# Performance work log

Measured on AMD Instinct MI355X. Metric: run time of the kernel, lower is better.

Reference implementation:

```python
import jax, jax.numpy as jnp
import numpy as np

N_AGT, N_CTX, E, D, NC = 100000, 10000, 1000000, 128, 2


def _gn(x, w, b, eps=1e-5):
    # GroupNorm(num_groups=1) on (N, C): normalize over channels, affine.
    m = jnp.mean(x, axis=-1, keepdims=True)
    v = jnp.mean((x - m) ** 2, axis=-1, keepdims=True)
    return (x - m) * jax.lax.rsqrt(v + eps) * w + b


def setup_inputs() -> dict:
    key = jax.random.key(0)
    ks = jax.random.split(key, 16)
    s = 0.05  # weight scale
    return {
        "agts": jax.random.normal(ks[0], (N_AGT, D), jnp.float32),
        "ctx": jax.random.normal(ks[1], (N_CTX, D), jnp.float32),
        "agt_ctrs": jax.random.normal(ks[2], (N_AGT, NC), jnp.float32),
        "ctx_ctrs": jax.random.normal(ks[3], (N_CTX, NC), jnp.float32),
        "hi": jax.random.randint(ks[4], (E,), 0, N_AGT, jnp.int32),
        "wi": jax.random.randint(ks[5], (E,), 0, N_CTX, jnp.int32),
        "dist_w1": jax.random.normal(ks[6], (D, NC), jnp.float32) * s,
        "dist_b1": jnp.zeros((D,), jnp.float32),
        "dist_w2": jax.random.normal(ks[7], (D, D), jnp.float32) * s,
        "dist_gw": jnp.ones((D,), jnp.float32),
        "dist_gb": jnp.zeros((D,), jnp.float32),
        "q_w": jax.random.normal(ks[8], (D, D), jnp.float32) * s,
        "q_gw": jnp.ones((D,), jnp.float32),
        "q_gb": jnp.zeros((D,), jnp.float32),
        "ctx_w1": jax.random.normal(ks[9], (D, 3 * D), jnp.float32) * s,
        "ctx_gw": jnp.ones((D,), jnp.float32),
        "ctx_gb": jnp.zeros((D,), jnp.float32),
        "ctx_w2": jax.random.normal(ks[10], (D, D), jnp.float32) * s,
        "agt_w": jax.random.normal(ks[11], (D, D), jnp.float32) * s,
        "norm_gw": jnp.ones((D,), jnp.float32),
        "norm_gb": jnp.zeros((D,), jnp.float32),
        "lin_w": jax.random.normal(ks[12], (D, D), jnp.float32) * s,
        "lin_gw": jnp.ones((D,), jnp.float32),
        "lin_gb": jnp.zeros((D,), jnp.float32),
    }


def reference(agts, ctx, agt_ctrs, ctx_ctrs, hi, wi,
              dist_w1, dist_b1, dist_w2, dist_gw, dist_gb,
              q_w, q_gw, q_gb,
              ctx_w1, ctx_gw, ctx_gb, ctx_w2,
              agt_w, norm_gw, norm_gb,
              lin_w, lin_gw, lin_gb):
    res = agts
    # per-edge relative displacement: [E, 2]
    d = agt_ctrs[hi] - ctx_ctrs[wi]
    # dist MLP: Linear(2,128)+ReLU, Linear(128,128,nobias)+GN+ReLU
    d = jax.nn.relu(d @ dist_w1.T + dist_b1)
    d = jax.nn.relu(_gn(d @ dist_w2.T, dist_gw, dist_gb))
    # query: Linear(128,128,nobias)+GN+ReLU on gathered agents
    q = jax.nn.relu(_gn(agts[hi] @ q_w.T, q_gw, q_gb))
    # concat-MLP over edges: [E, 384] -> [E, 128]
    c = jnp.concatenate([d, q, ctx[wi]], axis=1)
    c = jax.nn.relu(_gn(c @ ctx_w1.T, ctx_gw, ctx_gb))
    c = c @ ctx_w2.T
    # agent transform + index_add scatter of edge messages
    a = agts @ agt_w.T
    a = a.at[hi].add(c)
    a = jax.nn.relu(_gn(a, norm_gw, norm_gb))
    a = _gn(a @ lin_w.T, lin_gw, lin_gb)  # Linear block with act=False
    a = jax.nn.relu(a + res)
    return a
```

## Files before the change

### kernel.cpp

```cpp
#include <hip/hip_runtime.h>
#include <stdint.h>


#define N_AGT 100000
#define N_CTX 10000
#define NE    1000000
#define D     128

typedef __attribute__((ext_vector_type(8))) __bf16 bf16x8;
typedef __attribute__((ext_vector_type(4))) float f32x4;
typedef __attribute__((ext_vector_type(4))) unsigned int uint32x4;
typedef __attribute__((ext_vector_type(8))) unsigned short ushort8;

__device__ __forceinline__ float bf_lo(uint32_t u){ return __uint_as_float(u << 16); }
__device__ __forceinline__ float bf_hi(uint32_t u){ return __uint_as_float(u & 0xFFFF0000u); }
__device__ __forceinline__ uint16_t f2bf(float f){
  uint32_t u = __float_as_uint(f);
  u += 0x7FFFu + ((u >> 16) & 1u);
  return (uint16_t)(u >> 16);
}
__device__ __forceinline__ float bf2f(uint16_t v){ return __uint_as_float(((uint32_t)v) << 16); }

__device__ __forceinline__ f32x4 mfma16(bf16x8 a, bf16x8 b, f32x4 c){
  return __builtin_amdgcn_mfma_f32_16x16x32_bf16(a, b, c, 0, 0, 0);
}

__device__ __forceinline__ void wave_lgkm0(){
  asm volatile("s_waitcnt lgkmcnt(0)" ::: "memory");
  __builtin_amdgcn_sched_barrier(0);
}


__device__ __forceinline__ void stage_wsz(char* dst, const float* __restrict__ W,
                                          int rs, int co, int tid, int nthr){
  for (int idx = tid; idx < 128*16; idx += nthr){
    const int row = idx >> 4, ch = idx & 15;
    const float4 f0 = *(const float4*)(W + (size_t)row*rs + co + ch*8);
    const float4 f1 = *(const float4*)(W + (size_t)row*rs + co + ch*8 + 4);
    ushort8 u;
    u[0]=f2bf(f0.x); u[1]=f2bf(f0.y); u[2]=f2bf(f0.z); u[3]=f2bf(f0.w);
    u[4]=f2bf(f1.x); u[5]=f2bf(f1.y); u[6]=f2bf(f1.z); u[7]=f2bf(f1.w);
    *(uint32x4*)(dst + row*256 + ((ch*16) ^ ((row&7)<<4))) = __builtin_bit_cast(uint32x4, u);
  }
}

__device__ __forceinline__ bf16x8 ldfrag(const char* base, int row, int cb){
  return __builtin_bit_cast(bf16x8,
      *(const uint32x4*)(base + row*256 + (cb ^ ((row&7)<<4))));
}

#define NWIT (NE/16)

__device__ __forceinline__ void mm16(const char* T, const char* W,
                                     int llo, int lhi, f32x4 acc[8]){
  bf16x8 a[4];
  #pragma unroll
  for (int kt = 0; kt < 4; kt++) a[kt] = ldfrag(T, llo, kt*64 + lhi*16);
  #pragma unroll
  for (int nt = 0; nt < 8; nt++){
    acc[nt] = (f32x4)0.f;
    #pragma unroll
    for (int kt = 0; kt < 4; kt++){
      const bf16x8 b = ldfrag(W, nt*16 + llo, kt*64 + lhi*16);
      acc[nt] = mfma16(a[kt], b, acc[nt]);
    }
  }
}

__device__ __forceinline__ void gn_reg(f32x4 acc[8], const float gw[8],
                                       const float gb[8]){
  float s[4] = {0,0,0,0}, ss[4] = {0,0,0,0};
  #pragma unroll
  for (int nt = 0; nt < 8; nt++)
    #pragma unroll
    for (int r = 0; r < 4; r++){
      const float v = acc[nt][r];
      s[r] += v; ss[r] += v*v;
    }
  #pragma unroll
  for (int m = 1; m < 16; m <<= 1)
    #pragma unroll
    for (int r = 0; r < 4; r++){
      s[r] += __shfl_xor(s[r], m);
      ss[r] += __shfl_xor(ss[r], m);
    }
  float mean[4], rstd[4];
  #pragma unroll
  for (int r = 0; r < 4; r++){
    mean[r] = s[r]*(1.f/128.f);
    const float var = ss[r]*(1.f/128.f) - mean[r]*mean[r];
    rstd[r] = rsqrtf(var + 1e-5f);
  }
  #pragma unroll
  for (int nt = 0; nt < 8; nt++)
    #pragma unroll
    for (int r = 0; r < 4; r++)
      acc[nt][r] = fmaxf((acc[nt][r]-mean[r])*rstd[r]*gw[nt] + gb[nt], 0.f);
}

__device__ __forceinline__ void scat16(char* T, const f32x4 acc[8],
                                       int llo, int lhi){
  #pragma unroll
  for (int nt = 0; nt < 8; nt++)
    #pragma unroll
    for (int r = 0; r < 4; r++){
      const int row = lhi*4 + r;
      *(uint16_t*)(T + row*256 + ((2*(nt*16 + llo)) ^ ((row&7)<<4))) =
          f2bf(acc[nt][r]);
    }
}

__global__ __launch_bounds__(512, 2) void k_edge_mfma(
    const float* __restrict__ agt_ctrs, const float* __restrict__ ctx_ctrs,
    const int* __restrict__ hi, const int* __restrict__ wi,
    const float* __restrict__ dist_w1, const float* __restrict__ dist_b1,
    const float* __restrict__ dist_gw, const float* __restrict__ dist_gb,
    const float* __restrict__ ctx_gw, const float* __restrict__ ctx_gb,
    const float* __restrict__ dist_w2, const float* __restrict__ ctx_w1,
    const float* __restrict__ ctx_w2,
    const uint16_t* __restrict__ QW, const uint16_t* __restrict__ CtxP,
    float* __restrict__ A0){
  extern __shared__ __align__(16) char smem[];
  const int tid  = threadIdx.x;
  const int wave = tid >> 6, lane = tid & 63;
  const int lhi  = lane >> 4, llo = lane & 15;

  stage_wsz(smem,         dist_w2, 128, 0, tid, 512);
  stage_wsz(smem + 32768, ctx_w1,  384, 0, tid, 512);
  stage_wsz(smem + 65536, ctx_w2,  128, 0, tid, 512);

  char* T = smem + 98304 + wave*4096;

  const int c0 = llo*8;
  float w1x[8], w1y[8], b1v[8];
  #pragma unroll
  for (int j = 0; j < 8; j++){
    w1x[j] = dist_w1[(c0+j)*2 + 0];
    w1y[j] = dist_w1[(c0+j)*2 + 1];
    b1v[j] = dist_b1[c0+j];
  }
  float dgwr[8], dgbr[8], cgwr[8], cgbr[8];
  #pragma unroll
  for (int nt = 0; nt < 8; nt++){
    dgwr[nt] = dist_gw[nt*16 + llo]; dgbr[nt] = dist_gb[nt*16 + llo];
    cgwr[nt] = ctx_gw[nt*16 + llo];  cgbr[nt] = ctx_gb[nt*16 + llo];
  }
  __syncthreads();

  const int wid = blockIdx.x*8 + wave;
  const int nw  = gridDim.x*8;

  for (int i = wid; i < NWIT; i += nw){
    const int base = i*16;
    const int4 h4 = *(const int4*)&hi[base + lhi*4];
    const int4 w4 = *(const int4*)&wi[base + lhi*4];
    const int hh[4] = {h4.x, h4.y, h4.z, h4.w};
    const int ww[4] = {w4.x, w4.y, w4.z, w4.w};
    const int h2 = hi[base + llo], w2 = wi[base + llo];
    uint32x4 qql[4], qcl[4];
    #pragma unroll
    for (int k = 0; k < 4; k++){
      qql[k] = *(const uint32x4*)&QW  [(size_t)h2*D + lhi*32 + k*8];
      qcl[k] = *(const uint32x4*)&CtxP[(size_t)w2*D + lhi*32 + k*8];
    }
    #pragma unroll
    for (int j = 0; j < 4; j++){
      const float2 ac = *(const float2*)&agt_ctrs[(size_t)hh[j]*2];
      const float2 cc = *(const float2*)&ctx_ctrs[(size_t)ww[j]*2];
      const float dx = ac.x - cc.x, dy = ac.y - cc.y;
      ushort8 u;
      #pragma unroll
      for (int c = 0; c < 8; c++)
        u[c] = f2bf(fmaxf(fmaf(dx, w1x[c], fmaf(dy, w1y[c], b1v[c])), 0.f));
      const int row = lhi*4 + j;
      *(uint32x4*)(T + row*256 + ((llo*16) ^ ((row&7)<<4))) =
          __builtin_bit_cast(uint32x4, u);
    }
    wave_lgkm0();
    f32x4 acc[8];
    mm16(T, smem, llo, lhi, acc);
    gn_reg(acc, dgwr, dgbr);
    wave_lgkm0();
    scat16(T, acc, llo, lhi);
    wave_lgkm0();
    mm16(T, smem + 32768, llo, lhi, acc);
    ushort8 qs[4];
    #pragma unroll
    for (int k = 0; k < 4; k++){
      const ushort8 a = __builtin_bit_cast(ushort8, qql[k]);
      const ushort8 b = __builtin_bit_cast(ushort8, qcl[k]);
      ushort8 v;
      #pragma unroll
      for (int j = 0; j < 8; j++) v[j] = f2bf(bf2f(a[j]) + bf2f(b[j]));
      qs[k] = v;
    }
    wave_lgkm0();
    #pragma unroll
    for (int k = 0; k < 4; k++)
      *(uint32x4*)(T + llo*256 + (((lhi*64) + k*16) ^ ((llo&7)<<4))) =
          __builtin_bit_cast(uint32x4, qs[k]);
    wave_lgkm0();
    #pragma unroll
    for (int nt = 0; nt < 8; nt++)
      #pragma unroll
      for (int r = 0; r < 4; r++){
        const int row = lhi*4 + r;
        const uint16_t q = *(const uint16_t*)(T + row*256 +
            ((2*(nt*16 + llo)) ^ ((row&7)<<4)));
        acc[nt][r] += bf2f(q);
      }
    gn_reg(acc, cgwr, cgbr);
    wave_lgkm0();
    scat16(T, acc, llo, lhi);
    wave_lgkm0();
    mm16(T, smem + 65536, llo, lhi, acc);
    #pragma unroll
    for (int nt = 0; nt < 8; nt++)
      #pragma unroll
      for (int r = 0; r < 4; r++)
        atomicAdd(&A0[(size_t)hh[r]*D + nt*16 + llo], acc[nt][r]);
  }
}

__device__ __forceinline__ void mm_stage(const char* xb, const char* wm, int wv,
                                         int llo, int lhi, f32x4 acc[3][2]){
  #pragma unroll
  for (int kt = 0; kt < 4; kt++){
    const int cb = kt*64 + lhi*16;
    const bf16x8 b0 = ldfrag(wm, wv*32 + llo,      cb);
    const bf16x8 b1 = ldfrag(wm, wv*32 + 16 + llo, cb);
    #pragma unroll
    for (int mt = 0; mt < 3; mt++){
      const bf16x8 a = ldfrag(xb, mt*16 + llo, cb);
      acc[mt][0] = mfma16(a, b0, acc[mt][0]);
      acc[mt][1] = mfma16(a, b1, acc[mt][1]);
    }
  }
}

__device__ __forceinline__ void scat_acc(char* xb, const f32x4 acc[3][2],
                                         int wv, int llo, int lhi){
  #pragma unroll
  for (int mt = 0; mt < 3; mt++)
    #pragma unroll
    for (int ntl = 0; ntl < 2; ntl++)
      #pragma unroll
      for (int r = 0; r < 4; r++){
        const int m = mt*16 + lhi*4 + r;
        const int n = wv*32 + ntl*16 + llo;
        *(uint16_t*)(xb + m*256 + ((n*2) ^ ((m&7)<<4))) = f2bf(acc[mt][ntl][r]);
      }
}

__device__ __forceinline__ void gn_rowpass(char* xb, const int rr[3], int llo,
                                           const float gw[8], const float gb[8]){
  #pragma unroll
  for (int i = 0; i < 3; i++){
    const int row = rr[i];
    char* p = xb + row*256 + ((llo*16) ^ ((row&7)<<4));
    ushort8 u = __builtin_bit_cast(ushort8, *(const uint32x4*)p);
    float f[8]; float s = 0.f, ss = 0.f;
    #pragma unroll
    for (int j = 0; j < 8; j++){ f[j] = bf2f(u[j]); s += f[j]; ss += f[j]*f[j]; }
    #pragma unroll
    for (int m = 1; m < 16; m <<= 1){ s += __shfl_xor(s, m); ss += __shfl_xor(ss, m); }
    const float mean = s*(1.f/128.f);
    const float var  = ss*(1.f/128.f) - mean*mean;
    const float rstd = rsqrtf(var + 1e-5f);
    #pragma unroll
    for (int j = 0; j < 8; j++){
      const float g = fmaxf((f[j]-mean)*rstd*gw[j] + gb[j], 0.f);
      u[j] = f2bf(g);
    }
    *(uint32x4*)p = __builtin_bit_cast(uint32x4, u);
  }
}

#define NITER_A ((N_AGT + 95) / 96)

__global__ __launch_bounds__(512, 2) void k_agent_pre_mfma(
    const float* __restrict__ agts, const float* __restrict__ q_w,
    const float* __restrict__ ctx_w1, const float* __restrict__ agt_w,
    const float* __restrict__ q_gw, const float* __restrict__ q_gb,
    uint16_t* __restrict__ QW, float* __restrict__ A0){
  extern __shared__ __align__(16) char smem[];
  const int tid  = threadIdx.x;
  const int wave = tid >> 6, lane = tid & 63;
  const int grp  = wave >> 2, wv = wave & 3;
  const int lhi  = lane >> 4, llo = lane & 15;

  stage_wsz(smem,         q_w,    128, 0,   tid, 512);
  stage_wsz(smem + 32768, agt_w,  128, 0,   tid, 512);
  stage_wsz(smem + 65536, ctx_w1, 384, 128, tid, 512);

  char* xb = smem + 98304 + grp*12288;
  const int c0 = llo*8;
  float qgw[8], qgb[8];
  #pragma unroll
  for (int j = 0; j < 8; j++){ qgw[j] = q_gw[c0+j]; qgb[j] = q_gb[c0+j]; }
  __syncthreads();

  const int tg = tid & 255;
  int rr[3];
  #pragma unroll
  for (int i = 0; i < 3; i++) rr[i] = wv*12 + i*4 + lhi;

  for (int it = blockIdx.x; it < NITER_A; it += gridDim.x){
    const int rbase = it*96 + grp*48;
    for (int idx = tg; idx < 48*32; idx += 256){
      const int row = idx >> 5, c4 = idx & 31;
      int gr = rbase + row; if (gr >= N_AGT) gr = N_AGT - 1;
      const float4 f = *(const float4*)(agts + (size_t)gr*D + c4*4);
      const uint32_t lo = ((uint32_t)f2bf(f.y) << 16) | (uint32_t)f2bf(f.x);
      const uint32_t hi2 = ((uint32_t)f2bf(f.w) << 16) | (uint32_t)f2bf(f.z);
      *(uint2*)(xb + row*256 + ((c4*8) ^ ((row&7)<<4))) = make_uint2(lo, hi2);
    }
    __syncthreads();
    f32x4 acc[3][2];
    #pragma unroll
    for (int mt = 0; mt < 3; mt++){ acc[mt][0] = (f32x4)0.f; acc[mt][1] = (f32x4)0.f; }
    mm_stage(xb, smem + 32768, wv, llo, lhi, acc);
    #pragma unroll
    for (int mt = 0; mt < 3; mt++)
      #pragma unroll
      for (int ntl = 0; ntl < 2; ntl++)
        #pragma unroll
        for (int r = 0; r < 4; r++){
          const int m = mt*16 + lhi*4 + r;
          if (rbase + m < N_AGT){
            const int n = wv*32 + ntl*16 + llo;
            A0[(size_t)(rbase + m)*D + n] = acc[mt][ntl][r];
          }
        }
    #pragma unroll
    for (int mt = 0; mt < 3; mt++){ acc[mt][0] = (f32x4)0.f; acc[mt][1] = (f32x4)0.f; }
    mm_stage(xb, smem, wv, llo, lhi, acc);
    __syncthreads();
    scat_acc(xb, acc, wv, llo, lhi);
    __syncthreads();
    gn_rowpass(xb, rr, llo, qgw, qgb);
    __syncthreads();
    #pragma unroll
    for (int mt = 0; mt < 3; mt++){ acc[mt][0] = (f32x4)0.f; acc[mt][1] = (f32x4)0.f; }
    mm_stage(xb, smem + 65536, wv, llo, lhi, acc);
    __syncthreads();
    scat_acc(xb, acc, wv, llo, lhi);
    __syncthreads();
    #pragma unroll
    for (int i = 0; i < 3; i++){
      const int row = rr[i], gr = rbase + row;
      if (gr < N_AGT){
        const uint32x4 u = *(const uint32x4*)(xb + row*256 + ((llo*16) ^ ((row&7)<<4)));
        *(uint32x4*)(QW + (size_t)gr*D + c0) = u;
      }
    }
    __syncthreads();
  }
}

__global__ __launch_bounds__(512, 4) void k_post_mfma(
    float* __restrict__ A0, const float* __restrict__ agts,
    const float* __restrict__ lin_w,
    const float* __restrict__ norm_gw, const float* __restrict__ norm_gb,
    const float* __restrict__ lin_gw, const float* __restrict__ lin_gb){
  extern __shared__ __align__(16) char smem[];
  const int tid  = threadIdx.x;
  const int wave = tid >> 6, lane = tid & 63;
  const int grp  = wave >> 2, wv = wave & 3;
  const int lhi  = lane >> 4, llo = lane & 15;

  stage_wsz(smem, lin_w, 128, 0, tid, 512);
  char* xb = smem + 32768 + grp*12288;
  const int c0 = llo*8;
  float ngw[8], ngb[8], lgw[8], lgb[8];
  #pragma unroll
  for (int j = 0; j < 8; j++){
    ngw[j] = norm_gw[c0+j]; ngb[j] = norm_gb[c0+j];
    lgw[j] = lin_gw[c0+j];  lgb[j] = lin_gb[c0+j];
  }
  __syncthreads();

  int rr[3];
  #pragma unroll
  for (int i = 0; i < 3; i++) rr[i] = wv*12 + i*4 + lhi;

  for (int it = blockIdx.x; it < NITER_A; it += gridDim.x){
    const int rbase = it*96 + grp*48;
    #pragma unroll
    for (int i = 0; i < 3; i++){
      const int row = rr[i];
      int gr = rbase + row; if (gr >= N_AGT) gr = N_AGT - 1;
      const float4 a0 = *(const float4*)(A0 + (size_t)gr*D + c0);
      const float4 a1 = *(const float4*)(A0 + (size_t)gr*D + c0 + 4);
      float f[8] = {a0.x,a0.y,a0.z,a0.w,a1.x,a1.y,a1.z,a1.w};
      float s = 0.f, ss = 0.f;
      #pragma unroll
      for (int j = 0; j < 8; j++){ s += f[j]; ss += f[j]*f[j]; }
      #pragma unroll
      for (int m = 1; m < 16; m <<= 1){ s += __shfl_xor(s, m); ss += __shfl_xor(ss, m); }
      const float mean = s*(1.f/128.f);
      const float var  = ss*(1.f/128.f) - mean*mean;
      const float rstd = rsqrtf(var + 1e-5f);
      ushort8 u;
      #pragma unroll
      for (int j = 0; j < 8; j++)
        u[j] = f2bf(fmaxf((f[j]-mean)*rstd*ngw[j] + ngb[j], 0.f));
      *(uint32x4*)(xb + row*256 + ((llo*16) ^ ((row&7)<<4))) =
          __builtin_bit_cast(uint32x4, u);
    }
    __syncthreads();
    f32x4 acc[3][2];
    #pragma unroll
    for (int mt = 0; mt < 3; mt++){ acc[mt][0] = (f32x4)0.f; acc[mt][1] = (f32x4)0.f; }
    mm_stage(xb, smem, wv, llo, lhi, acc);
    __syncthreads();
    scat_acc(xb, acc, wv, llo, lhi);
    __syncthreads();
    #pragma unroll
    for (int i = 0; i < 3; i++){
      const int row = rr[i];
      const char* p = xb + row*256 + ((llo*16) ^ ((row&7)<<4));
      const ushort8 u = __builtin_bit_cast(ushort8, *(const uint32x4*)p);
      float f[8]; float s = 0.f, ss = 0.f;
      #pragma unroll
      for (int j = 0; j < 8; j++){ f[j] = bf2f(u[j]); s += f[j]; ss += f[j]*f[j]; }
      #pragma unroll
      for (int m = 1; m < 16; m <<= 1){ s += __shfl_xor(s, m); ss += __shfl_xor(ss, m); }
      const float mean = s*(1.f/128.f);
      const float var  = ss*(1.f/128.f) - mean*mean;
      const float rstd = rsqrtf(var + 1e-5f);
      const int gr = rbase + row;
      if (gr < N_AGT){
        const float4 r0 = *(const float4*)(agts + (size_t)gr*D + c0);
        const float4 r1 = *(const float4*)(agts + (size_t)gr*D + c0 + 4);
        const float res[8] = {r0.x,r0.y,r0.z,r0.w,r1.x,r1.y,r1.z,r1.w};
        float o[8];
        float4 o0, o1;
        #pragma unroll
        for (int j = 0; j < 8; j++)
          o[j] = fmaxf((f[j]-mean)*rstd*lgw[j] + lgb[j] + res[j], 0.f);
        o0.x=o[0]; o0.y=o[1]; o0.z=o[2]; o0.w=o[3];
        o1.x=o[4]; o1.y=o[5]; o1.z=o[6]; o1.w=o[7];
        *(float4*)(A0 + (size_t)gr*D + c0)     = o0;
        *(float4*)(A0 + (size_t)gr*D + c0 + 4) = o1;
      }
    }
    __syncthreads();
  }
}

__device__ __forceinline__ void stage_w4(uint32_t* wp, const float* __restrict__ W,
                                         int rs, int co, int tid, int nthr){
  for (int idx = tid; idx < 32*128; idx += nthr){
    int p2 = idx & 31, o = idx >> 5;
    const float4 f = *(const float4*)(W + (size_t)o*rs + co + p2*4);
    uint32_t lo = ((uint32_t)f2bf(f.y) << 16) | (uint32_t)f2bf(f.x);
    uint32_t hi = ((uint32_t)f2bf(f.w) << 16) | (uint32_t)f2bf(f.z);
    *(uint2*)&wp[(p2*128 + o)*2] = make_uint2(lo, hi);
  }
}

__device__ __forceinline__ float dot128(const uint32_t* wp, const float* xb, int o){
  float acc = 0.f;
  #pragma unroll 8
  for (int p2 = 0; p2 < 32; p2++){
    const uint2 w = *(const uint2*)&wp[(p2*128 + o)*2];
    const float4 x = *(const float4*)&xb[p2*4];
    acc += x.x*bf_lo(w.x) + x.y*bf_hi(w.x) + x.z*bf_lo(w.y) + x.w*bf_hi(w.y);
  }
  return acc;
}

__global__ __launch_bounds__(128) void k_ctx(const float* __restrict__ ctx,
                                             const float* __restrict__ ctx_w1,
                                             uint16_t* __restrict__ CtxP){
  __shared__ __align__(16) uint32_t wc[32*128*2];
  __shared__ __align__(16) float xbuf[128];
  const int tid = threadIdx.x;
  stage_w4(wc, ctx_w1, 384, 256, tid, 128);
  __syncthreads();
  for (int row = blockIdx.x; row < N_CTX; row += gridDim.x){
    __syncthreads();
    xbuf[tid] = ctx[(size_t)row*D + tid];
    __syncthreads();
    const float acc = dot128(wc, xbuf, tid);
    CtxP[(size_t)row*D + tid] = f2bf(acc);
  }
}

extern "C" void kernel_launch(void* const* d_in, const int* in_sizes, int n_in,
                              void* d_out, int out_size, void* d_ws, size_t ws_size,
                              hipStream_t stream){
  const float* agts     = (const float*)d_in[0];
  const float* ctx      = (const float*)d_in[1];
  const float* agt_ctrs = (const float*)d_in[2];
  const float* ctx_ctrs = (const float*)d_in[3];
  const int*   hi       = (const int*)d_in[4];
  const int*   wi       = (const int*)d_in[5];
  const float* dist_w1  = (const float*)d_in[6];
  const float* dist_b1  = (const float*)d_in[7];
  const float* dist_w2  = (const float*)d_in[8];
  const float* dist_gw  = (const float*)d_in[9];
  const float* dist_gb  = (const float*)d_in[10];
  const float* q_w      = (const float*)d_in[11];
  const float* q_gw     = (const float*)d_in[12];
  const float* q_gb     = (const float*)d_in[13];
  const float* ctx_w1   = (const float*)d_in[14];
  const float* ctx_gw   = (const float*)d_in[15];
  const float* ctx_gb   = (const float*)d_in[16];
  const float* ctx_w2   = (const float*)d_in[17];
  const float* agt_w    = (const float*)d_in[18];
  const float* norm_gw  = (const float*)d_in[19];
  const float* norm_gb  = (const float*)d_in[20];
  const float* lin_w    = (const float*)d_in[21];
  const float* lin_gw   = (const float*)d_in[22];
  const float* lin_gb   = (const float*)d_in[23];

  uint16_t* QW   = (uint16_t*)d_ws;
  uint16_t* CtxP = QW + (size_t)N_AGT * D;
  float*    A0   = (float*)d_out;

  const int EDGE_LDS = 131072;
  const int APRE_LDS = 122880;
  const int POST_LDS = 57344;
  hipFuncSetAttribute((const void*)k_edge_mfma,
                      hipFuncAttributeMaxDynamicSharedMemorySize, EDGE_LDS);
  hipFuncSetAttribute((const void*)k_agent_pre_mfma,
                      hipFuncAttributeMaxDynamicSharedMemorySize, APRE_LDS);
  hipFuncSetAttribute((const void*)k_post_mfma,
                      hipFuncAttributeMaxDynamicSharedMemorySize, POST_LDS);

  k_ctx<<<1024, 128, 0, stream>>>(ctx, ctx_w1, CtxP);
  k_agent_pre_mfma<<<256, 512, APRE_LDS, stream>>>(agts, q_w, ctx_w1, agt_w,
      q_gw, q_gb, QW, A0);
  k_edge_mfma<<<256, 512, EDGE_LDS, stream>>>(agt_ctrs, ctx_ctrs, hi, wi,
      dist_w1, dist_b1, dist_gw, dist_gb, ctx_gw, ctx_gb,
      dist_w2, ctx_w1, ctx_w2, QW, CtxP, A0);
  k_post_mfma<<<512, 512, POST_LDS, stream>>>(A0, agts, lin_w,
      norm_gw, norm_gb, lin_gw, lin_gb);
}
```

Baseline: 614.1 us.

## Sort edges by destination agent and segment-reduce messages before atomics

Adds a counting sort of edges by target agent (histogram, single-block scan, scatter) so the edge kernel walks edges grouped by hi. In the edge kernel, each 16-edge tile's output goes through LDS and is summed over runs of equal agent index before atomicAdd, cutting per-edge float atomics to one per run. This adds three extra kernels, a memset and a serial 1024-thread scan. With random indices, runs within a 16-edge tile are short (about 10 edges per agent on average), and the scatter pass itself issues 1M atomics.

```diff
diff --git a/kernel.cpp b/kernel.cpp
--- a/kernel.cpp
+++ b/kernel.cpp
@@ -49,6 +49,48 @@
       *(const uint32x4*)(base + row*256 + (cb ^ ((row&7)<<4))));
 }
 
+__global__ __launch_bounds__(256) void k_hist(const int* __restrict__ hi,
+                                              int* __restrict__ cnt){
+  for (int i = blockIdx.x*256 + threadIdx.x; i < NE; i += gridDim.x*256)
+    atomicAdd(&cnt[hi[i]], 1);
+}
+
+__global__ __launch_bounds__(1024) void k_scan(int* __restrict__ cnt){
+  __shared__ int part[1024];
+  const int t = threadIdx.x;
+  const int chunk = (N_AGT + 1023) / 1024;
+  const int lo = t*chunk, hi2 = min(lo + chunk, N_AGT);
+  int s = 0;
+  for (int i = lo; i < hi2; i++) s += cnt[i];
+  part[t] = s;
+  __syncthreads();
+  for (int ofs = 1; ofs < 1024; ofs <<= 1){
+    int add = (t >= ofs) ? part[t - ofs] : 0;
+    __syncthreads();
+    part[t] += add;
+    __syncthreads();
+  }
+  int run = part[t] - s;
+  for (int i = lo; i < hi2; i++){
+    const int c = cnt[i];
+    cnt[i] = run;
+    run += c;
+  }
+}
+
+__global__ __launch_bounds__(256) void k_scatter(const int* __restrict__ hi,
+                                                 const int* __restrict__ wi,
+                                                 int* __restrict__ cur,
+                                                 int* __restrict__ hs,
+                                                 int* __restrict__ ws){
+  for (int i = blockIdx.x*256 + threadIdx.x; i < NE; i += gridDim.x*256){
+    const int h = hi[i];
+    const int pos = atomicAdd(&cur[h], 1);
+    hs[pos] = h;
+    ws[pos] = wi[i];
+  }
+}
+
 #define NWIT (NE/16)
 
 __device__ __forceinline__ void mm16(const char* T, const char* W,
@@ -112,7 +154,7 @@
 
 __global__ __launch_bounds__(512, 2) void k_edge_mfma(
     const float* __restrict__ agt_ctrs, const float* __restrict__ ctx_ctrs,
-    const int* __restrict__ hi, const int* __restrict__ wi,
+    const int* __restrict__ hs, const int* __restrict__ ws,
     const float* __restrict__ dist_w1, const float* __restrict__ dist_b1,
     const float* __restrict__ dist_gw, const float* __restrict__ dist_gb,
     const float* __restrict__ ctx_gw, const float* __restrict__ ctx_gb,
@@ -152,11 +194,11 @@
 
   for (int i = wid; i < NWIT; i += nw){
     const int base = i*16;
-    const int4 h4 = *(const int4*)&hi[base + lhi*4];
-    const int4 w4 = *(const int4*)&wi[base + lhi*4];
+    const int4 h4 = *(const int4*)&hs[base + lhi*4];
+    const int4 w4 = *(const int4*)&ws[base + lhi*4];
     const int hh[4] = {h4.x, h4.y, h4.z, h4.w};
     const int ww[4] = {w4.x, w4.y, w4.z, w4.w};
-    const int h2 = hi[base + llo], w2 = wi[base + llo];
+    const int h2 = hs[base + llo], w2 = ws[base + llo];
     uint32x4 qql[4], qcl[4];
     #pragma unroll
     for (int k = 0; k < 4; k++){
@@ -214,11 +256,27 @@
     scat16(T, acc, llo, lhi);
     wave_lgkm0();
     mm16(T, smem + 65536, llo, lhi, acc);
-    #pragma unroll
-    for (int nt = 0; nt < 8; nt++)
-      #pragma unroll
-      for (int r = 0; r < 4; r++)
-        atomicAdd(&A0[(size_t)hh[r]*D + nt*16 + llo], acc[nt][r]);
+    wave_lgkm0();
+    scat16(T, acc, llo, lhi);
+    wave_lgkm0();
+    {
+      const int cA = lane, cB = lane + 64;
+      float runA = 0.f, runB = 0.f;
+      int hprev = __shfl(h2, 0);
+      #pragma unroll
+      for (int k = 0; k < 16; k++){
+        const int hk = __shfl(h2, k);
+        if (hk != hprev){
+          atomicAdd(&A0[(size_t)hprev*D + cA], runA);
+          atomicAdd(&A0[(size_t)hprev*D + cB], runB);
+          runA = 0.f; runB = 0.f; hprev = hk;
+        }
+        runA += bf2f(*(const uint16_t*)(T + k*256 + ((2*cA) ^ ((k&7)<<4))));
+        runB += bf2f(*(const uint16_t*)(T + k*256 + ((2*cB) ^ ((k&7)<<4))));
+      }
+      atomicAdd(&A0[(size_t)hprev*D + cA], runA);
+      atomicAdd(&A0[(size_t)hprev*D + cB], runB);
+    }
   }
 }
 
@@ -518,6 +576,9 @@
 
   uint16_t* QW   = (uint16_t*)d_ws;
   uint16_t* CtxP = QW + (size_t)N_AGT * D;
+  int*      cnt  = (int*)((char*)d_ws + 28160000);
+  int*      hs   = (int*)((char*)d_ws + 28560000);
+  int*      wss  = (int*)((char*)d_ws + 32560000);
   float*    A0   = (float*)d_out;
 
   const int EDGE_LDS = 131072;
@@ -530,10 +591,15 @@
   hipFuncSetAttribute((const void*)k_post_mfma,
                       hipFuncAttributeMaxDynamicSharedMemorySize, POST_LDS);
 
+  hipMemsetAsync(cnt, 0, (size_t)N_AGT*4, stream);
+  k_hist<<<2048, 256, 0, stream>>>(hi, cnt);
+  k_scan<<<1, 1024, 0, stream>>>(cnt);
+  k_scatter<<<2048, 256, 0, stream>>>(hi, wi, cnt, hs, wss);
+
   k_ctx<<<1024, 128, 0, stream>>>(ctx, ctx_w1, CtxP);
   k_agent_pre_mfma<<<256, 512, APRE_LDS, stream>>>(agts, q_w, ctx_w1, agt_w,
       q_gw, q_gb, QW, A0);
-  k_edge_mfma<<<256, 512, EDGE_LDS, stream>>>(agt_ctrs, ctx_ctrs, hi, wi,
+  k_edge_mfma<<<256, 512, EDGE_LDS, stream>>>(agt_ctrs, ctx_ctrs, hs, wss,
       dist_w1, dist_b1, dist_gw, dist_gb, ctx_gw, ctx_gb,
       dist_w2, ctx_w1, ctx_w2, QW, CtxP, A0);
   k_post_mfma<<<512, 512, POST_LDS, stream>>>(A0, agts, lin_w,
```

New measurement: 726.5 us. 1.18x slower.
